# Optimization experiments

Measured on AMD Instinct MI355X. Metric: run time of the kernel, lower is better.

The kernel has to match this reference:

```python
import jax, jax.numpy as jnp
import numpy as np

B, S, D, H, DK, HID = 2, 2048, 768, 12, 64, 3072
EPS = 1e-5

def layernorm(x, g, b):
    mu = jnp.mean(x, axis=-1, keepdims=True)
    var = jnp.var(x, axis=-1, keepdims=True)
    return (x - mu) * jax.lax.rsqrt(var + EPS) * g + b

def setup_inputs() -> dict:
    key = jax.random.key(0)
    ks = jax.random.split(key, 9)
    std = 0.02
    x = jax.random.normal(ks[0], (B, S, D), dtype=jnp.float32)
    Wq = jax.random.normal(ks[1], (H, D, DK), dtype=jnp.float32) * std
    Wk = jax.random.normal(ks[2], (H, D, DK), dtype=jnp.float32) * std
    Wv = jax.random.normal(ks[3], (H, D, DK), dtype=jnp.float32) * std
    Wo = jax.random.normal(ks[4], (H * DK, D), dtype=jnp.float32) * std
    W1 = jax.random.normal(ks[5], (D, HID), dtype=jnp.float32) * std
    b1 = jnp.zeros((HID,), dtype=jnp.float32)
    W2 = jax.random.normal(ks[6], (HID, D), dtype=jnp.float32) * std
    b2 = jnp.zeros((D,), dtype=jnp.float32)
    g_ln1 = jnp.ones((D,), dtype=jnp.float32)
    b_ln1 = jnp.zeros((D,), dtype=jnp.float32)
    g_ln2 = jnp.ones((D,), dtype=jnp.float32)
    b_ln2 = jnp.zeros((D,), dtype=jnp.float32)
    return {"x": x, "Wq": Wq, "Wk": Wk, "Wv": Wv, "Wo": Wo,
            "W1": W1, "b1": b1, "W2": W2, "b2": b2,
            "g_ln1": g_ln1, "b_ln1": b_ln1, "g_ln2": g_ln2, "b_ln2": b_ln2}

def reference(x, Wq, Wk, Wv, Wo, W1, b1, W2, b2, g_ln1, b_ln1, g_ln2, b_ln2):
    seq = x.shape[1]
    h = layernorm(x, g_ln1, b_ln1)
    # per-head projections, vectorized over heads: [B,H,S,DK]
    Q = jnp.einsum('bsd,hdk->bhsk', h, Wq)
    K = jnp.einsum('bsd,hdk->bhsk', h, Wk)
    V = jnp.einsum('bsd,hdk->bhsk', h, Wv)
    scores = jnp.einsum('bhsk,bhtk->bhst', Q, K) / jnp.sqrt(jnp.float32(DK))
    mask = jnp.triu(jnp.full((seq, seq), -jnp.inf, dtype=scores.dtype), k=1)
    A = jax.nn.softmax(scores + mask, axis=-1)
    out = jnp.einsum('bhst,bhtk->bhsk', A, V)  # [B,H,S,DK]
    # concat heads (matches torch.cat over heads dim=-1)
    out = out.transpose(0, 2, 1, 3).reshape(x.shape[0], seq, H * DK)
    attn = out @ Wo
    y = x + attn
    h2 = layernorm(y, g_ln2, b_ln2)
    mlp = jax.nn.gelu(h2 @ W1 + b1, approximate=False) @ W2 + b2
    return y + mlp
```

## Files before the change

### kernel.cpp

```cpp
#include <hip/hip_runtime.h>
#include <hip/hip_bf16.h>
#include <cstdint>
#include <cstddef>

using bf16 = __hip_bfloat16;
typedef __attribute__((ext_vector_type(8))) short short8;
typedef __attribute__((ext_vector_type(4))) float f32x4;
typedef __attribute__((ext_vector_type(2))) int i32x2;

#define DEV static __device__ __forceinline__

#define MROWS 4096
#define SEQ   2048
#define DMODEL 768
#define NHEAD 12
#define DHEAD 64
#define HID   3072
#define QSCALE 0.1803368801111204f

DEV void gload16(const void* g, void* l) {
  __builtin_amdgcn_global_load_lds((const __attribute__((address_space(1))) void*)g,
                                   (__attribute__((address_space(3))) void*)l, 16, 0, 0);
}

template <int CTRL>
DEV float dppf(float x) {
  return __builtin_bit_cast(float,
      __builtin_amdgcn_mov_dpp(__builtin_bit_cast(int, x), CTRL, 0xF, 0xF, true));
}
DEV float red_add16(float x) {
  x += dppf<0xB1>(x);
  x += dppf<0x4E>(x);
  x += dppf<0x141>(x);
  x += dppf<0x140>(x);
  return x;
}

DEV float gelu_exact(float x) {
  float z = fabsf(x) * 0.70710678118f;
  float t = __builtin_amdgcn_rcpf(fmaf(0.3275911f, z, 1.0f));
  float poly = fmaf(1.061405429f, t, -1.453152027f);
  poly = fmaf(poly, t, 1.421413741f);
  poly = fmaf(poly, t, -0.284496736f);
  poly = fmaf(poly, t, 0.254829592f);
  poly *= t;
  float e = __builtin_amdgcn_exp2f(-0.72134752044f * x * x);
  float erfv = fmaf(-poly, e, 1.0f);
  erfv = copysignf(erfv, x);
  return 0.5f * x * (1.0f + erfv);
}

__global__ __launch_bounds__(256) void cvt_qkv_k(const float* __restrict__ Wq,
                                                 const float* __restrict__ Wk,
                                                 const float* __restrict__ Wv,
                                                 bf16* __restrict__ out) {
  int idx = blockIdx.x * 256 + threadIdx.x;
  int n = idx / DMODEL, d = idx - n * DMODEL;
  int proj = n / DMODEL;
  int within = n - proj * DMODEL;
  int hh = within >> 6, k = within & 63;
  const float* W = (proj == 0) ? Wq : (proj == 1 ? Wk : Wv);
  out[idx] = __float2bfloat16(W[((size_t)hh * DMODEL + d) * DHEAD + k]);
}

__global__ __launch_bounds__(256) void cvt_t_k(const float* __restrict__ W,
                                               bf16* __restrict__ out, int R, int C) {
  int idx = blockIdx.x * 256 + threadIdx.x;
  int c = idx / R, r = idx - c * R;
  out[idx] = __float2bfloat16(W[(size_t)r * C + c]);
}

__global__ __launch_bounds__(256) void ln_k(const float* __restrict__ in,
                                            const float* __restrict__ gam,
                                            const float* __restrict__ bet,
                                            bf16* __restrict__ out) {
  int r = blockIdx.x;
  int tid = threadIdx.x;
  const float* p = in + (size_t)r * DMODEL;
  float v0 = p[tid], v1 = p[tid + 256], v2 = p[tid + 512];
  float s = v0 + v1 + v2;
  float ss = v0 * v0 + v1 * v1 + v2 * v2;
#pragma unroll
  for (int off = 1; off < 64; off <<= 1) {
    s += __shfl_xor(s, off);
    ss += __shfl_xor(ss, off);
  }
  __shared__ float rs[4], rss[4];
  int w = tid >> 6, l = tid & 63;
  if (l == 0) { rs[w] = s; rss[w] = ss; }
  __syncthreads();
  s = rs[0] + rs[1] + rs[2] + rs[3];
  ss = rss[0] + rss[1] + rss[2] + rss[3];
  float mean = s * (1.0f / 768.0f);
  float var = ss * (1.0f / 768.0f) - mean * mean;
  float inv = rsqrtf(var + 1e-5f);
  bf16* o = out + (size_t)r * DMODEL;
  o[tid]       = __float2bfloat16((v0 - mean) * inv * gam[tid] + bet[tid]);
  o[tid + 256] = __float2bfloat16((v1 - mean) * inv * gam[tid + 256] + bet[tid + 256]);
  o[tid + 512] = __float2bfloat16((v2 - mean) * inv * gam[tid + 512] + bet[tid + 512]);
}

template <int EPI>
DEV void gemm_epilogue(int r, int c, float v,
                       bf16* __restrict__ ob, float* __restrict__ of,
                       const float* __restrict__ add, const float* __restrict__ bias,
                       bf16* __restrict__ vt) {
  if constexpr (EPI == 0) {
    if (c < 1536) {
      float scv = (c < DMODEL) ? QSCALE : 1.0f;
      ob[(size_t)r * 1536 + c] = __float2bfloat16(v * scv);
    } else {
      int within = c - 1536;
      int hh = within >> 6, kk = within & 63;
      int bidx = r >> 11, sq = r & 2047;
      int sqp = (sq & ~63) | ((sq & 15) << 2) | ((sq >> 4) & 3);
      vt[(((size_t)bidx * NHEAD + hh) * DHEAD + kk) * SEQ + sqp] = __float2bfloat16(v);
    }
  } else if constexpr (EPI == 1) {
    of[(size_t)r * DMODEL + c] = add[(size_t)r * DMODEL + c] + v;
  } else if constexpr (EPI == 2) {
    ob[(size_t)r * HID + c] = __float2bfloat16(gelu_exact(v + bias[c]));
  } else {
    of[(size_t)r * DMODEL + c] = add[(size_t)r * DMODEL + c] + v + bias[c];
  }
}

template <int EPI, int BM, int BN>
__global__ __launch_bounds__(256) void gemm_bt(const bf16* __restrict__ A,
                                               const bf16* __restrict__ Bt, int K,
                                               bf16* __restrict__ ob,
                                               float* __restrict__ of,
                                               const float* __restrict__ add,
                                               const float* __restrict__ bias,
                                               bf16* __restrict__ vt) {
  __shared__ bf16 sA[2][BM * 32];
  __shared__ bf16 sB[2][BN * 32];
  constexpr int MI = BM / 32;
  constexpr int NI = BN / 32;
  constexpr int LOADS = (BM == 128 ? 2 : 1) + (BN == 128 ? 2 : 1);
  const int tid = threadIdx.x;
  const int w = tid >> 6, l = tid & 63;
  const int lr = l & 15, lg = l >> 4;
  const int mbase = blockIdx.y * BM, nbase = blockIdx.x * BN;
  const int wm = (w >> 1) * (BM / 2), wn = (w & 1) * (BN / 2);

  f32x4 acc[MI][NI];
#pragma unroll
  for (int i = 0; i < MI; ++i)
#pragma unroll
    for (int j = 0; j < NI; ++j) acc[i][j] = (f32x4)0.0f;

  const int srow = l >> 2;
  const int scol = ((l & 3) ^ ((l >> 3) & 3)) * 8;
  const bf16* gA = A + (size_t)(mbase + (BM == 128 ? w * 32 : w * 16) + srow) * K + scol;
  const bf16* gB = Bt + (size_t)(nbase + (BN == 128 ? w * 32 : w * 16) + srow) * K + scol;
  const int foff = (lg ^ ((lr >> 1) & 3)) * 8;

#define GSTAGE(bufi, t)                                                      \
  {                                                                          \
    const int k0_ = (t) * 32;                                                \
    if constexpr (BM == 128) {                                               \
      gload16(gA + k0_, &sA[bufi][w * 1024]);                                \
      gload16(gA + k0_ + (size_t)16 * K, &sA[bufi][w * 1024 + 512]);         \
    } else {                                                                 \
      gload16(gA + k0_, &sA[bufi][w * 512]);                                 \
    }                                                                        \
    if constexpr (BN == 128) {                                               \
      gload16(gB + k0_, &sB[bufi][w * 1024]);                                \
      gload16(gB + k0_ + (size_t)16 * K, &sB[bufi][w * 1024 + 512]);         \
    } else {                                                                 \
      gload16(gB + k0_, &sB[bufi][w * 512]);                                 \
    }                                                                        \
  }

  const int nt = K >> 5;
  GSTAGE(0, 0);
  for (int t = 0; t < nt; ++t) {
    const int cur = t & 1;
    if (t + 1 < nt) {
      GSTAGE(cur ^ 1, t + 1);
      if constexpr (LOADS == 4)      asm volatile("s_waitcnt vmcnt(4)" ::: "memory");
      else if constexpr (LOADS == 3) asm volatile("s_waitcnt vmcnt(3)" ::: "memory");
      else                           asm volatile("s_waitcnt vmcnt(2)" ::: "memory");
    } else {
      asm volatile("s_waitcnt vmcnt(0)" ::: "memory");
    }
    __builtin_amdgcn_s_barrier();

    short8 a[MI], bb[NI];
#pragma unroll
    for (int mi = 0; mi < MI; ++mi)
      a[mi] = *(const short8*)&sA[cur][(wm + mi * 16 + lr) * 32 + foff];
#pragma unroll
    for (int ni = 0; ni < NI; ++ni)
      bb[ni] = *(const short8*)&sB[cur][(wn + ni * 16 + lr) * 32 + foff];
#pragma unroll
    for (int mi = 0; mi < MI; ++mi)
#pragma unroll
      for (int ni = 0; ni < NI; ++ni)
        acc[mi][ni] = __builtin_amdgcn_mfma_f32_16x16x32_bf16(a[mi], bb[ni], acc[mi][ni], 0, 0, 0);

    __builtin_amdgcn_s_barrier();
  }
#undef GSTAGE

  const int row0 = mbase + wm + lg * 4;
  const int col0 = nbase + wn + lr;
#pragma unroll
  for (int mi = 0; mi < MI; ++mi)
#pragma unroll
    for (int ni = 0; ni < NI; ++ni)
#pragma unroll
      for (int i = 0; i < 4; ++i)
        gemm_epilogue<EPI>(row0 + mi * 16 + i, col0 + ni * 16, acc[mi][ni][i],
                           ob, of, add, bias, vt);
}

template <int EPI>
__global__ __launch_bounds__(256) void gemm64_bt(const bf16* __restrict__ A,
                                                 const bf16* __restrict__ Bt, int K,
                                                 bf16* __restrict__ ob,
                                                 float* __restrict__ of,
                                                 const float* __restrict__ add,
                                                 const float* __restrict__ bias) {
  __shared__ bf16 sA[2][64 * 64];
  __shared__ bf16 sB[2][64 * 64];
  const int tid = threadIdx.x;
  const int w = tid >> 6, l = tid & 63;
  const int lr = l & 15, lg = l >> 4;
  const int mbase = blockIdx.y * 64, nbase = blockIdx.x * 64;
  const int wm = (w >> 1) * 32, wn = (w & 1) * 32;

  f32x4 acc[2][2];
#pragma unroll
  for (int i = 0; i < 2; ++i)
#pragma unroll
    for (int j = 0; j < 2; ++j) acc[i][j] = (f32x4)0.0f;

  const int srow3 = l >> 3;
  const int csrc = ((l & 7) ^ srow3) * 8;
  const bf16* gA = A + (size_t)(mbase + w * 16 + srow3) * K + csrc;
  const bf16* gB = Bt + (size_t)(nbase + w * 16 + srow3) * K + csrc;

  int rowa[2], rowb[2], cswz[2];
#pragma unroll
  for (int mi = 0; mi < 2; ++mi) rowa[mi] = (wm + mi * 16 + lr) * 64;
#pragma unroll
  for (int ni = 0; ni < 2; ++ni) rowb[ni] = (wn + ni * 16 + lr) * 64;
#pragma unroll
  for (int kk = 0; kk < 2; ++kk) cswz[kk] = (((kk * 4 + lg) ^ (lr & 7)) << 3);

#define GSTAGE64(bufi, t)                                                    \
  {                                                                          \
    const int k0_ = (t) * 64;                                                \
    gload16(gA + k0_,                 &sA[bufi][(w * 16) * 64]);             \
    gload16(gA + k0_ + (size_t)8 * K, &sA[bufi][(w * 16 + 8) * 64]);         \
    gload16(gB + k0_,                 &sB[bufi][(w * 16) * 64]);             \
    gload16(gB + k0_ + (size_t)8 * K, &sB[bufi][(w * 16 + 8) * 64]);         \
  }

  const int nt = K >> 6;
  GSTAGE64(0, 0);
  for (int t = 0; t < nt; ++t) {
    const int cur = t & 1;
    if (t + 1 < nt) {
      GSTAGE64(cur ^ 1, t + 1);
      asm volatile("s_waitcnt vmcnt(4)" ::: "memory");
    } else {
      asm volatile("s_waitcnt vmcnt(0)" ::: "memory");
    }
    __builtin_amdgcn_s_barrier();

    short8 a[2][2], bb[2][2];
#pragma unroll
    for (int mi = 0; mi < 2; ++mi)
#pragma unroll
      for (int kk = 0; kk < 2; ++kk)
        a[mi][kk] = *(const short8*)&sA[cur][rowa[mi] + cswz[kk]];
#pragma unroll
    for (int ni = 0; ni < 2; ++ni)
#pragma unroll
      for (int kk = 0; kk < 2; ++kk)
        bb[ni][kk] = *(const short8*)&sB[cur][rowb[ni] + cswz[kk]];
#pragma unroll
    for (int mi = 0; mi < 2; ++mi)
#pragma unroll
      for (int ni = 0; ni < 2; ++ni) {
        acc[mi][ni] = __builtin_amdgcn_mfma_f32_16x16x32_bf16(a[mi][0], bb[ni][0], acc[mi][ni], 0, 0, 0);
        acc[mi][ni] = __builtin_amdgcn_mfma_f32_16x16x32_bf16(a[mi][1], bb[ni][1], acc[mi][ni], 0, 0, 0);
      }

    __builtin_amdgcn_s_barrier();
  }
#undef GSTAGE64

  const int row0 = mbase + wm + lg * 4;
  const int col0 = nbase + wn + lr;
#pragma unroll
  for (int mi = 0; mi < 2; ++mi)
#pragma unroll
    for (int ni = 0; ni < 2; ++ni)
#pragma unroll
      for (int i = 0; i < 4; ++i)
        gemm_epilogue<EPI>(row0 + mi * 16 + i, col0 + ni * 16, acc[mi][ni][i],
                           ob, of, add, bias, nullptr);
}

__global__ __launch_bounds__(256) void attn_k(const bf16* __restrict__ qk,
                                              const bf16* __restrict__ vt,
                                              bf16* __restrict__ o) {
  __shared__ bf16 sK[2][64 * 64];
  __shared__ bf16 sV[2][64 * 64];
  __shared__ bf16 sP[64 * 64];

  const int d = blockIdx.x;
  const int bh = d % 24;
  const int qt = 31 - d / 24;
  const int b = bh / NHEAD, h = bh - b * NHEAD;
  const int qbase = qt * 64;
  const int tid = threadIdx.x, w = tid >> 6, l = tid & 63;
  const int lr = l & 15, lg = l >> 4;

  short8 q[2];
#pragma unroll
  for (int kk = 0; kk < 2; ++kk)
    q[kk] = *(const short8*)&qk[(size_t)(b * SEQ + qbase + w * 16 + lr) * 1536 + h * DHEAD + kk * 32 + lg * 8];

  f32x4 oa[4];
  float lst[4];
#pragma unroll
  for (int i = 0; i < 4; ++i) { oa[i] = (f32x4)0.0f; lst[i] = 0.0f; }

  const int srow3 = l >> 3;
  const int csrc = (l & 7) ^ srow3;
  const bf16* gKb = qk + ((size_t)(b * SEQ) + w * 16 + srow3) * 1536 + DMODEL + h * DHEAD + csrc * 8;
  const bf16* gVb = vt + ((size_t)bh * DHEAD + w * 16 + srow3) * SEQ + csrc * 8;

  int rowb[4], cswz[2];
#pragma unroll
  for (int ni = 0; ni < 4; ++ni) rowb[ni] = (ni * 16 + lr) * 64;
#pragma unroll
  for (int kk = 0; kk < 2; ++kk) cswz[kk] = (((kk * 4 + lg) ^ (lr & 7)) << 3);
  const int prow = (w * 16 + lr) * 64;

#define STAGE(buf, t)                                                              \
  {                                                                                \
    const int kb_ = (t) * 64;                                                      \
    gload16(gKb + (size_t)kb_ * 1536,        &sK[buf][(w * 16) * 64]);             \
    gload16(gKb + (size_t)(kb_ + 8) * 1536,  &sK[buf][(w * 16 + 8) * 64]);         \
    gload16(gVb + kb_,                       &sV[buf][(w * 16) * 64]);             \
    gload16(gVb + kb_ + (size_t)8 * SEQ,     &sV[buf][(w * 16 + 8) * 64]);         \
  }

  STAGE(0, 0);

  for (int t = 0; t <= qt; ++t) {
    const int cur = t & 1;
    const int kb = t * 64;
    if (t < qt) {
      STAGE(cur ^ 1, t + 1);
      asm volatile("s_waitcnt vmcnt(4)" ::: "memory");
    } else {
      asm volatile("s_waitcnt vmcnt(0)" ::: "memory");
    }
    __builtin_amdgcn_s_barrier();

    const bf16* sKc = sK[cur];
    const bf16* sVc = sV[cur];

    f32x4 sc[4];
    __builtin_amdgcn_s_setprio(1);
#pragma unroll
    for (int ni = 0; ni < 4; ++ni) {
      sc[ni] = (f32x4)0.0f;
#pragma unroll
      for (int kk = 0; kk < 2; ++kk) {
        short8 kf = *(const short8*)&sKc[rowb[ni] + cswz[kk]];
        sc[ni] = __builtin_amdgcn_mfma_f32_16x16x32_bf16(q[kk], kf, sc[ni], 0, 0, 0);
      }
    }
    __builtin_amdgcn_s_setprio(0);

    const bool need_mask = (kb + 63) > (qbase + w * 16);
    const int qrow0 = qbase + w * 16 + lg * 4;
#pragma unroll
    for (int i = 0; i < 4; ++i) {
      float v0 = sc[0][i], v1 = sc[1][i], v2 = sc[2][i], v3 = sc[3][i];
      if (need_mask) {
        const int qg = qrow0 + i;
        v0 = (kb + lr      > qg) ? -1e30f : v0;
        v1 = (kb + 16 + lr > qg) ? -1e30f : v1;
        v2 = (kb + 32 + lr > qg) ? -1e30f : v2;
        v3 = (kb + 48 + lr > qg) ? -1e30f : v3;
      }
      float p0 = exp2f(v0), p1 = exp2f(v1), p2 = exp2f(v2), p3 = exp2f(v3);
      lst[i] += (p0 + p1) + (p2 + p3);
      int r0, r1;
      asm("v_cvt_pk_bf16_f32 %0, %1, %2" : "=v"(r0) : "v"(p0), "v"(p1));
      asm("v_cvt_pk_bf16_f32 %0, %1, %2" : "=v"(r1) : "v"(p2), "v"(p3));
      const int rrow = w * 16 + lg * 4 + i;
      *(i32x2*)((char*)sP + rrow * 128 + ((lr * 8) ^ ((rrow & 7) << 4))) = (i32x2){r0, r1};
    }

    short8 pf0 = *(const short8*)&sP[prow + cswz[0]];
    short8 pf1 = *(const short8*)&sP[prow + cswz[1]];
    __builtin_amdgcn_s_setprio(1);
#pragma unroll
    for (int nk = 0; nk < 4; ++nk) {
      short8 vf0 = *(const short8*)&sVc[rowb[nk] + cswz[0]];
      short8 vf1 = *(const short8*)&sVc[rowb[nk] + cswz[1]];
      oa[nk] = __builtin_amdgcn_mfma_f32_16x16x32_bf16(pf0, vf0, oa[nk], 0, 0, 0);
      oa[nk] = __builtin_amdgcn_mfma_f32_16x16x32_bf16(pf1, vf1, oa[nk], 0, 0, 0);
    }
    __builtin_amdgcn_s_setprio(0);
    __builtin_amdgcn_s_barrier();
  }
#undef STAGE

#pragma unroll
  for (int i = 0; i < 4; ++i) lst[i] = red_add16(lst[i]);
#pragma unroll
  for (int i = 0; i < 4; ++i) {
    const float rl = __builtin_amdgcn_rcpf(lst[i]);
#pragma unroll
    for (int nk = 0; nk < 4; ++nk) {
      int row = qbase + w * 16 + lg * 4 + i;
      int col = h * DHEAD + nk * 16 + lr;
      o[(size_t)(b * SEQ + row) * DMODEL + col] = __float2bfloat16(oa[nk][i] * rl);
    }
  }
}

extern "C" void kernel_launch(void* const* d_in, const int* in_sizes, int n_in,
                              void* d_out, int out_size, void* d_ws, size_t ws_size,
                              hipStream_t stream) {
  (void)in_sizes; (void)n_in; (void)out_size; (void)ws_size;
  const float* x   = (const float*)d_in[0];
  const float* Wq  = (const float*)d_in[1];
  const float* Wk  = (const float*)d_in[2];
  const float* Wv  = (const float*)d_in[3];
  const float* Wo  = (const float*)d_in[4];
  const float* W1  = (const float*)d_in[5];
  const float* b1  = (const float*)d_in[6];
  const float* W2  = (const float*)d_in[7];
  const float* b2  = (const float*)d_in[8];
  const float* g1  = (const float*)d_in[9];
  const float* be1 = (const float*)d_in[10];
  const float* g2  = (const float*)d_in[11];
  const float* be2 = (const float*)d_in[12];
  float* out = (float*)d_out;

  char* p = (char*)d_ws;
  bf16* WqkvT = (bf16*)p; p += (size_t)2304 * 768 * 2;
  bf16* WoT   = (bf16*)p; p += (size_t)768 * 768 * 2;
  bf16* W1T   = (bf16*)p; p += (size_t)3072 * 768 * 2;
  bf16* W2T   = (bf16*)p; p += (size_t)768 * 3072 * 2;
  bf16* h1    = (bf16*)p; p += (size_t)MROWS * DMODEL * 2;
  char* alias0 = p;
  bf16* QK    = (bf16*)p; p += (size_t)MROWS * 1536 * 2;
  bf16* Vt    = (bf16*)p; p += (size_t)24 * DHEAD * SEQ * 2;
  bf16* O     = (bf16*)p; p += (size_t)MROWS * DMODEL * 2;
  float* y    = (float*)p; p += (size_t)MROWS * DMODEL * 4;
  bf16* h2    = (bf16*)p; p += (size_t)MROWS * DMODEL * 2;
  bf16* U     = (bf16*)alias0;

  dim3 blk(256);
  cvt_qkv_k<<<(2304 * 768) / 256, blk, 0, stream>>>(Wq, Wk, Wv, WqkvT);
  cvt_t_k<<<(768 * 768) / 256, blk, 0, stream>>>(Wo, WoT, 768, 768);
  cvt_t_k<<<(768 * 3072) / 256, blk, 0, stream>>>(W1, W1T, 768, 3072);
  cvt_t_k<<<(3072 * 768) / 256, blk, 0, stream>>>(W2, W2T, 3072, 768);
  ln_k<<<MROWS, blk, 0, stream>>>(x, g1, be1, h1);
  gemm_bt<0, 128, 128><<<dim3(18, 32), blk, 0, stream>>>(h1, WqkvT, 768, QK, nullptr, nullptr, nullptr, Vt);
  attn_k<<<768, blk, 0, stream>>>(QK, Vt, O);
  gemm64_bt<1><<<dim3(12, 64), blk, 0, stream>>>(O, WoT, 768, nullptr, y, x, nullptr);
  ln_k<<<MROWS, blk, 0, stream>>>(y, g2, be2, h2);
  gemm64_bt<2><<<dim3(48, 64), blk, 0, stream>>>(h2, W1T, 768, U, nullptr, nullptr, b1);
  gemm64_bt<3><<<dim3(12, 64), blk, 0, stream>>>(U, W2T, 3072, nullptr, out, y, b2);
}
```

Measured before the change: 223.7 us.

## Split long causal attention query tiles across KV chunks with a combine kernel

Query tiles covering longer causal prefixes are now split into up to four KV-range chunks, so the attention grid grows from 768 to 1920 blocks of more even length. Split chunks write unnormalized fp32 partial outputs and row sums to workspace. A new combine kernel sums these partials and normalizes them into the bf16 output. The aim is to fix load imbalance and tail effects from triangular causal work. In exchange it adds a second launch and extra fp32 partial traffic through memory.

```diff
diff --git a/kernel.cpp b/kernel.cpp
--- a/kernel.cpp
+++ b/kernel.cpp
@@ -308,14 +308,26 @@
 
 __global__ __launch_bounds__(256) void attn_k(const bf16* __restrict__ qk,
                                               const bf16* __restrict__ vt,
-                                              bf16* __restrict__ o) {
+                                              bf16* __restrict__ o,
+                                              float* __restrict__ opart,
+                                              float* __restrict__ lpart) {
   __shared__ bf16 sK[2][64 * 64];
   __shared__ bf16 sV[2][64 * 64];
   __shared__ bf16 sP[64 * 64];
 
   const int d = blockIdx.x;
   const int bh = d % 24;
-  const int qt = 31 - d / 24;
+  const int rank = d / 24;
+  const int j = 79 - rank;
+  int qt, chunk, nch;
+  if (j < 8)       { qt = j;                        chunk = 0;           nch = 1; }
+  else if (j < 24) { int r_ = j - 8;  qt = 8  + (r_ >> 1); chunk = r_ & 1;  nch = 2; }
+  else if (j < 48) { int r_ = j - 24; qt = 16 + r_ / 3;    chunk = r_ % 3;  nch = 3; }
+  else             { int r_ = j - 48; qt = 24 + (r_ >> 2); chunk = r_ & 3;  nch = 4; }
+  const int nt_q = qt + 1;
+  const int t0 = (chunk * nt_q) / nch;
+  const int t1 = ((chunk + 1) * nt_q) / nch;
+
   const int b = bh / NHEAD, h = bh - b * NHEAD;
   const int qbase = qt * 64;
   const int tid = threadIdx.x, w = tid >> 6, l = tid & 63;
@@ -352,12 +364,12 @@
     gload16(gVb + kb_ + (size_t)8 * SEQ,     &sV[buf][(w * 16 + 8) * 64]);         \
   }
 
-  STAGE(0, 0);
-
-  for (int t = 0; t <= qt; ++t) {
-    const int cur = t & 1;
+  STAGE(0, t0);
+
+  for (int t = t0; t < t1; ++t) {
+    const int cur = (t - t0) & 1;
     const int kb = t * 64;
-    if (t < qt) {
+    if (t + 1 < t1) {
       STAGE(cur ^ 1, t + 1);
       asm volatile("s_waitcnt vmcnt(4)" ::: "memory");
     } else {
@@ -419,16 +431,65 @@
 
 #pragma unroll
   for (int i = 0; i < 4; ++i) lst[i] = red_add16(lst[i]);
-#pragma unroll
-  for (int i = 0; i < 4; ++i) {
-    const float rl = __builtin_amdgcn_rcpf(lst[i]);
-#pragma unroll
-    for (int nk = 0; nk < 4; ++nk) {
-      int row = qbase + w * 16 + lg * 4 + i;
-      int col = h * DHEAD + nk * 16 + lr;
-      o[(size_t)(b * SEQ + row) * DMODEL + col] = __float2bfloat16(oa[nk][i] * rl);
-    }
-  }
+
+  if (nch == 1) {
+#pragma unroll
+    for (int i = 0; i < 4; ++i) {
+      const float rl = __builtin_amdgcn_rcpf(lst[i]);
+#pragma unroll
+      for (int nk = 0; nk < 4; ++nk) {
+        int row = qbase + w * 16 + lg * 4 + i;
+        int col = h * DHEAD + nk * 16 + lr;
+        o[(size_t)(b * SEQ + row) * DMODEL + col] = __float2bfloat16(oa[nk][i] * rl);
+      }
+    }
+  } else {
+    const int slot = bh * 80 + j;
+    float* op = opart + (size_t)slot * 4096;
+#pragma unroll
+    for (int i = 0; i < 4; ++i) {
+      const int row = w * 16 + lg * 4 + i;
+#pragma unroll
+      for (int nk = 0; nk < 4; ++nk)
+        op[row * 64 + nk * 16 + lr] = oa[nk][i];
+      if (lr == 0) lpart[slot * 64 + row] = lst[i];
+    }
+  }
+}
+
+__global__ __launch_bounds__(256) void attn_comb_k(const float* __restrict__ opart,
+                                                   const float* __restrict__ lpart,
+                                                   bf16* __restrict__ o) {
+  const int s = blockIdx.x;
+  const int bh = s / 24;
+  const int qt = 8 + (s - bh * 24);
+  const int b = bh / NHEAD, h = bh - b * NHEAD;
+  const int bb = qt >> 3;
+  const int nch = bb + 1;
+  const int S0 = 4 * bb * (bb + 1) + (qt - 8 * bb) * (bb + 1);
+  const int slot0 = bh * 80 + S0;
+
+  const int tid = threadIdx.x;
+  const int row = tid >> 2;
+  const int c0 = (tid & 3) * 16;
+
+  f32x4 acc[4];
+#pragma unroll
+  for (int e = 0; e < 4; ++e) acc[e] = (f32x4)0.0f;
+  float lsum = 0.0f;
+  for (int c = 0; c < nch; ++c) {
+    const f32x4* op = (const f32x4*)(opart + (size_t)(slot0 + c) * 4096 + row * 64 + c0);
+    lsum += lpart[(slot0 + c) * 64 + row];
+#pragma unroll
+    for (int e = 0; e < 4; ++e) acc[e] += op[e];
+  }
+  const float rl = 1.0f / lsum;
+  bf16* po = o + (size_t)(b * SEQ + qt * 64 + row) * DMODEL + h * DHEAD + c0;
+#pragma unroll
+  for (int e = 0; e < 4; ++e)
+#pragma unroll
+    for (int k = 0; k < 4; ++k)
+      po[e * 4 + k] = __float2bfloat16(acc[e][k] * rl);
 }
 
 extern "C" void kernel_launch(void* const* d_in, const int* in_sizes, int n_in,
@@ -462,6 +523,8 @@
   bf16* O     = (bf16*)p; p += (size_t)MROWS * DMODEL * 2;
   float* y    = (float*)p; p += (size_t)MROWS * DMODEL * 4;
   bf16* h2    = (bf16*)p; p += (size_t)MROWS * DMODEL * 2;
+  float* Opart = (float*)p; p += (size_t)24 * 80 * 4096 * 4;
+  float* Lpart = (float*)p; p += (size_t)24 * 80 * 64 * 4;
   bf16* U     = (bf16*)alias0;
 
   dim3 blk(256);
@@ -471,7 +534,8 @@
   cvt_t_k<<<(3072 * 768) / 256, blk, 0, stream>>>(W2, W2T, 3072, 768);
   ln_k<<<MROWS, blk, 0, stream>>>(x, g1, be1, h1);
   gemm_bt<0, 128, 128><<<dim3(18, 32), blk, 0, stream>>>(h1, WqkvT, 768, QK, nullptr, nullptr, nullptr, Vt);
-  attn_k<<<768, blk, 0, stream>>>(QK, Vt, O);
+  attn_k<<<1920, blk, 0, stream>>>(QK, Vt, O, Opart, Lpart);
+  attn_comb_k<<<576, blk, 0, stream>>>(Opart, Lpart, O);
   gemm64_bt<1><<<dim3(12, 64), blk, 0, stream>>>(O, WoT, 768, nullptr, y, x, nullptr);
   ln_k<<<MROWS, blk, 0, stream>>>(y, g2, be2, h2);
   gemm64_bt<2><<<dim3(48, 64), blk, 0, stream>>>(h2, W1T, 768, U, nullptr, nullptr, b1);
```

After: 218.8 us. 2.2% less time.
